# Performance work log

Measured on AMD Instinct MI355X. Metric: run time of the kernel, lower is better.

The kernel has to match this reference:

```python
import jax, jax.numpy as jnp
import numpy as np

DIM = 2048
K = 8                 # top_k
M = 16                # max_transients
BIND_FRAC = 0.15
BETA = 0.05
GAMMA = 0.9
LIFETIME = 5
B, T = 64, 256

_iu, _ju = np.triu_indices(K, k=1)   # row-major: matches torch's (ii outer, jj inner) loop order
IU = jnp.asarray(_iu, jnp.int32)
JU = jnp.asarray(_ju, jnp.int32)


def _renorm(s):
    n = jnp.sqrt(jnp.sum(jnp.abs(s) ** 2, axis=-1, keepdims=True))
    return s / jnp.maximum(n, 1e-8)


def setup_inputs() -> dict:
    key = jax.random.key(0)
    ks = jax.random.split(key, 5)
    return {
        "x": jax.random.normal(ks[0], (B, T, DIM), jnp.float32),
        "tape_re": jax.random.normal(ks[1], (DIM,), jnp.float32) / np.sqrt(DIM).astype(np.float32),
        "tape_im": jax.random.normal(ks[2], (DIM,), jnp.float32) / np.sqrt(DIM).astype(np.float32),
        "eta_param": jnp.asarray(0.1, jnp.float32),
        "torque_bias_re": jax.random.normal(ks[3], (DIM,), jnp.float32) * 0.01,
        "torque_bias_im": jax.random.normal(ks[4], (DIM,), jnp.float32) * 0.01,
    }


def _per_batch(h, s, ti, tj, mre, mim, cnt, eta, tbias):
    """One timestep for one batch element. s: [D] complex64, transients: 5 arrays of [M]."""
    c = h * s                               # Hadamard reception
    _, top_idx = jax.lax.top_k(jnp.abs(c), K)
    top_c = c[top_idx]
    tm = jnp.abs(top_c)
    ph = jnp.angle(top_c)
    # co-resonance scores for the K*(K-1)/2 pairs; torch detaches via .item()
    score = jax.lax.stop_gradient(tm[IU] * tm[JU] * jnp.cos(ph[IU] - ph[JU]))
    pos = score > 0
    n_pos = jnp.sum(pos.astype(jnp.int32))
    n_bind = jnp.maximum(1, (n_pos.astype(jnp.float32) * BIND_FRAC).astype(jnp.int32))
    sorted_desc = -jnp.sort(-jnp.where(pos, score, -jnp.inf))
    theta_idx = jnp.minimum(n_bind - 1, jnp.maximum(n_pos - 1, 0))
    theta = sorted_desc[theta_idx]
    bind = (score >= theta) & (n_pos > 0)   # theta>0 so only positive scores pass

    ci = top_idx[IU]
    cj = top_idx[JU]
    prod = s[ci] * s[cj]
    mnew = jax.lax.stop_gradient(BETA * prod / jnp.maximum(jnp.abs(prod), 1e-8))  # torch detaches via .item()

    def step(tr, inp):
        ti, tj, mre, mim, cnt = tr
        ci_p, cj_p, do, mr, mi = inp
        active = cnt > 0
        match = active & (((ti == ci_p) & (tj == cj_p)) | ((ti == cj_p) & (tj == ci_p)))
        has_match = jnp.any(match)
        midx = jnp.argmax(match)
        free = ~active
        has_free = jnp.any(free)
        fidx = jnp.argmax(free)
        refresh = do & has_match
        insert = do & (~has_match) & has_free
        cnt = jnp.where(refresh, cnt.at[midx].set(LIFETIME), cnt)
        ti = jnp.where(insert, ti.at[fidx].set(ci_p), ti)
        tj = jnp.where(insert, tj.at[fidx].set(cj_p), tj)
        mre = jnp.where(insert, mre.at[fidx].set(mr), mre)
        mim = jnp.where(insert, mim.at[fidx].set(mi), mim)
        cnt = jnp.where(insert, cnt.at[fidx].set(LIFETIME), cnt)
        return (ti, tj, mre, mim, cnt), None

    (ti, tj, mre, mim, cnt), _ = jax.lax.scan(
        step, (ti, tj, mre, mim, cnt), (ci, cj, bind, mnew.real, mnew.imag))

    # decay all transients
    mre = mre * GAMMA
    mim = mim * GAMMA
    cnt = cnt - 1
    alive = (cnt > 0) & (jnp.sqrt(mre * mre + mim * mim) > 1e-6)
    cnt = jnp.where(alive, cnt, 0)
    mre = jnp.where(alive, mre, 0.0)
    mim = jnp.where(alive, mim, 0.0)

    # augment state with transients (scatter-add to both endpoints)
    s_re = s.real.at[ti].add(0.1 * mre).at[tj].add(0.1 * mre)
    s_im = s.imag.at[ti].add(0.1 * mim).at[tj].add(0.1 * mim)
    s_aug = jax.lax.complex(s_re, s_im)

    c_aug = h * s_aug
    re_c = c_aug.real
    im_c = c_aug.imag
    res_mask = ((re_c > 1e-6) & (jnp.abs(im_c) < re_c)).astype(jnp.float32)
    tor_mask = ((re_c < -1e-6) | (jnp.abs(im_c) >= jnp.abs(re_c))).astype(jnp.float32)
    orth_mask = 1.0 - res_mask - tor_mask
    update = eta * (c_aug * (1.0 - orth_mask) + tor_mask * tbias)
    s_new = _renorm(s + update)
    return s_new, ti, tj, mre, mim, cnt


def _forward(x, tape_re, tape_im, eta_param, torque_bias_re, torque_bias_im):
    Bb, Tt, D = x.shape
    s0 = _renorm(jax.lax.complex(tape_re, tape_im)[None, :])
    s0 = jnp.broadcast_to(s0, (Bb, D))
    eta = jnp.abs(eta_param)
    tbias = jax.lax.complex(torque_bias_re, torque_bias_im)
    ti0 = jnp.zeros((Bb, M), jnp.int32)
    tj0 = jnp.zeros((Bb, M), jnp.int32)
    mre0 = jnp.zeros((Bb, M), jnp.float32)
    mim0 = jnp.zeros((Bb, M), jnp.float32)
    cnt0 = jnp.zeros((Bb, M), jnp.int32)

    step_b = jax.vmap(_per_batch, in_axes=(0, 0, 0, 0, 0, 0, 0, None, None))

    def time_step(carry, h_t):
        s, ti, tj, mre, mim, cnt = carry
        s, ti, tj, mre, mim, cnt = step_b(h_t, s, ti, tj, mre, mim, cnt, eta, tbias)
        return (s, ti, tj, mre, mim, cnt), jnp.abs(s)

    _, outs = jax.lax.scan(time_step, (s0, ti0, tj0, mre0, mim0, cnt0),
                           jnp.transpose(x, (1, 0, 2)))  # [T,B,D]
    return jnp.transpose(outs, (1, 0, 2))                # [B,T,D]


def reference(x, tape_re, tape_im, eta_param, torque_bias_re, torque_bias_im):
    return _forward(x, tape_re, tape_im, eta_param, torque_bias_re, torque_bias_im)
```

## Files before the change

### kernel.cpp

```cpp
#include <hip/hip_runtime.h>
#include <math.h>

#define DIM_ 2048
#define KTOP 8
#define MSLOT 16
#define TSTEPS 256
#define NB 64
#define NTHREADS 320
#define NWORK 256
#define EPT 8
#define CCAP 128

static_assert(NWORK * EPT == DIM_, "mapping");

#define DPP0(src, ctrl, rm) __builtin_amdgcn_update_dpp(0, (src), (ctrl), (rm), 0xf, true)

__device__ __forceinline__ void ced(double &a, double &b) {
  double mx = fmax(a, b);
  b = fmin(a, b);
  a = mx;
}

template <int CTRL, int RM>
__device__ __forceinline__ void merge_2to4_d(double k[8]) {
  int lo0 = DPP0(__double2loint(k[0]), CTRL, RM);
  int hi0 = DPP0(__double2hiint(k[0]), CTRL, RM);
  int lo1 = DPP0(__double2loint(k[1]), CTRL, RM);
  int hi1 = DPP0(__double2hiint(k[1]), CTRL, RM);
  double b0 = __hiloint2double(hi0, lo0);
  double b1 = __hiloint2double(hi1, lo1);
  double z2 = b1, z3 = b0;
  ced(k[0], z2); ced(k[1], z3);
  ced(k[0], k[1]); ced(z2, z3);
  k[2] = z2; k[3] = z3;
}

template <int CTRL, int RM>
__device__ __forceinline__ void merge_first4(double k[8]) {
  double b[4];
#pragma unroll
  for (int i = 0; i < 4; i++) {
    int lo = DPP0(__double2loint(k[i]), CTRL, RM);
    int hi = DPP0(__double2hiint(k[i]), CTRL, RM);
    b[i] = __hiloint2double(hi, lo);
  }
  k[4] = b[3]; k[5] = b[2]; k[6] = b[1]; k[7] = b[0];
  ced(k[0],k[4]); ced(k[1],k[5]); ced(k[2],k[6]); ced(k[3],k[7]);
  ced(k[0],k[2]); ced(k[1],k[3]); ced(k[4],k[6]); ced(k[5],k[7]);
  ced(k[0],k[1]); ced(k[2],k[3]); ced(k[4],k[5]); ced(k[6],k[7]);
}

template <int CTRL, int RM>
__device__ __forceinline__ void merge_level(double k[8]) {
  double b[8];
#pragma unroll
  for (int i = 0; i < 8; i++) {
    int lo = DPP0(__double2loint(k[i]), CTRL, RM);
    int hi = DPP0(__double2hiint(k[i]), CTRL, RM);
    b[i] = __hiloint2double(hi, lo);
  }
#pragma unroll
  for (int i = 0; i < 8; i++) k[i] = fmax(k[i], b[7 - i]);
  ced(k[0],k[4]); ced(k[1],k[5]); ced(k[2],k[6]); ced(k[3],k[7]);
  ced(k[0],k[2]); ced(k[1],k[3]); ced(k[4],k[6]); ced(k[5],k[7]);
  ced(k[0],k[1]); ced(k[2],k[3]); ced(k[4],k[5]); ced(k[6],k[7]);
}

__device__ __forceinline__ void cedf(float &a, float &b) {
  float mx = fmaxf(a, b);
  b = fminf(a, b);
  a = mx;
}
__device__ __forceinline__ void sort4f(float k[8]) {
  cedf(k[0],k[1]); cedf(k[2],k[3]);
  cedf(k[0],k[2]); cedf(k[1],k[3]);
  cedf(k[1],k[2]);
}
template <int CTRL, int RM>
__device__ __forceinline__ void merge_first4_f32(float k[8]) {
  float b[4];
#pragma unroll
  for (int i = 0; i < 4; i++)
    b[i] = __int_as_float(DPP0(__float_as_int(k[i]), CTRL, RM));
  k[4] = b[3]; k[5] = b[2]; k[6] = b[1]; k[7] = b[0];
  cedf(k[0],k[4]); cedf(k[1],k[5]); cedf(k[2],k[6]); cedf(k[3],k[7]);
  cedf(k[0],k[2]); cedf(k[1],k[3]); cedf(k[4],k[6]); cedf(k[5],k[7]);
  cedf(k[0],k[1]); cedf(k[2],k[3]); cedf(k[4],k[5]); cedf(k[6],k[7]);
}
template <int CTRL, int RM>
__device__ __forceinline__ void merge_level_f32(float k[8]) {
  float b[8];
#pragma unroll
  for (int i = 0; i < 8; i++)
    b[i] = __int_as_float(DPP0(__float_as_int(k[i]), CTRL, RM));
#pragma unroll
  for (int i = 0; i < 8; i++) k[i] = fmaxf(k[i], b[7 - i]);
  cedf(k[0],k[4]); cedf(k[1],k[5]); cedf(k[2],k[6]); cedf(k[3],k[7]);
  cedf(k[0],k[2]); cedf(k[1],k[3]); cedf(k[4],k[6]); cedf(k[5],k[7]);
  cedf(k[0],k[1]); cedf(k[2],k[3]); cedf(k[4],k[5]); cedf(k[6],k[7]);
}

#define FMAX_STAGE(x, ctrl, rm)                                                \
  x = fmaxf(x, __int_as_float(DPP0(__float_as_int(x), ctrl, rm)))
#define FADD_STAGE(x, ctrl, rm)                                                \
  x = x + __int_as_float(DPP0(__float_as_int(x), ctrl, rm))

__device__ __forceinline__ float wave_max_f32(float x) {
  FMAX_STAGE(x, 0x111, 0xf);
  FMAX_STAGE(x, 0x112, 0xf);
  FMAX_STAGE(x, 0x114, 0xf);
  FMAX_STAGE(x, 0x118, 0xf);
  FMAX_STAGE(x, 0x142, 0xa);
  FMAX_STAGE(x, 0x143, 0xc);
  return x;
}
__device__ __forceinline__ float wave_sum_f32(float x) {
  FADD_STAGE(x, 0x111, 0xf);
  FADD_STAGE(x, 0x112, 0xf);
  FADD_STAGE(x, 0x114, 0xf);
  FADD_STAGE(x, 0x118, 0xf);
  FADD_STAGE(x, 0x142, 0xa);
  FADD_STAGE(x, 0x143, 0xc);
  return x;
}
__device__ __forceinline__ int rl63(int v) {
  return __builtin_amdgcn_readlane(v, 63);
}

__global__ void __launch_bounds__(NTHREADS)
me_fused(const float *__restrict__ x, const float *__restrict__ tape_re,
         const float *__restrict__ tape_im, const float *__restrict__ eta_param,
         const float *__restrict__ tbias_re, const float *__restrict__ tbias_im,
         float *__restrict__ out) {
  __shared__ float4 sc4[DIM_];
  __shared__ float2 dxy[DIM_];
  __shared__ float4 lmax4[NWORK / 4];
  __shared__ unsigned long long cand_lds[CCAP];
  __shared__ int ccnt;
  __shared__ float red_sh[4];

  const int tid = threadIdx.x;
  const int lane = tid & 63;
  const int wid = tid >> 6;
  const int wtid = tid - 64;
  const int b = blockIdx.x;

  const float eta = fabsf(eta_param[0]);

  float vre[EPT], vim[EPT], tbre_[EPT], tbim_[EPT];
  float hcur[EPT], hnext[EPT], av[EPT];
  const float *xb = x + (size_t)b * TSTEPS * DIM_;

  if (wid > 0) {
    float acc = 0.f, lm = 0.f;
#pragma unroll
    for (int j = 0; j < EPT; j++) {
      int e = wtid + NWORK * j;
      float a = tape_re[e], c2 = tape_im[e];
      vre[j] = a; vim[j] = c2;
      tbre_[j] = tbias_re[e]; tbim_[j] = tbias_im[e];
      float h = xb[e];
      hcur[j] = h; hnext[j] = h;
      dxy[e] = make_float2(0.f, 0.f);
      acc += a * a + c2 * c2;
      float cr = h * a, ci = h * c2;
      av[j] = sqrtf(cr * cr + ci * ci);
      lm = fmaxf(lm, av[j]);
      sc4[e] = make_float4(h, a, c2, 0.f);
    }
    float ws = wave_sum_f32(acc);
    if (lane == 63) red_sh[wid - 1] = ws;
    ((float *)lmax4)[wtid] = lm;
  }
  if (tid == 0) ccnt = 0;

  int s_ti = 0, s_tj = 0, s_cnt = 0;
  float s_mre = 0.f, s_mim = 0.f;

  float osr[EPT], osi[EPT];

  __syncthreads();

  for (int t = 0; t < TSTEPS; t++) {
    float ivn;
    {
      float tot = (red_sh[0] + red_sh[1]) + (red_sh[2] + red_sh[3]);
      ivn = 1.f / fmaxf(sqrtf(tot), 1e-8f);
    }

    if (wid > 0) {
      float4 q = lmax4[lane];
      float k[8];
      k[0] = q.x; k[1] = q.y; k[2] = q.z; k[3] = q.w;
      k[4] = 0.f; k[5] = 0.f; k[6] = 0.f; k[7] = 0.f;
      sort4f(k);
      merge_first4_f32<0x111, 0xf>(k);
      merge_level_f32<0x112, 0xf>(k);
      merge_level_f32<0x114, 0xf>(k);
      merge_level_f32<0x118, 0xf>(k);
      merge_level_f32<0x142, 0xa>(k);
      merge_level_f32<0x143, 0xc>(k);
      float th = __int_as_float(rl63(__float_as_int(k[7])));
#pragma unroll
      for (int j = 0; j < EPT; j++) {
        if (av[j] >= th) {
          int e = wtid + NWORK * j;
          int slot = atomicAdd(&ccnt, 1);
          if (slot < CCAP)
            cand_lds[slot] = (unsigned long long)__double_as_longlong(
                __hiloint2double(__float_as_int(av[j]), ~e));
        }
      }
    }
    __syncthreads();

    if (wid == 0) {
      int cnt = ccnt;
      if (lane == 0) ccnt = 0;
      if (cnt > CCAP) cnt = CCAP;
      unsigned long long u0 = cand_lds[2 * lane];
      unsigned long long u1 = cand_lds[2 * lane + 1];
      double a = (2 * lane < cnt) ? __longlong_as_double((long long)u0) : 0.0;
      double b2 = (2 * lane + 1 < cnt) ? __longlong_as_double((long long)u1) : 0.0;
      double c[8];
      c[0] = fmax(a, b2); c[1] = fmin(a, b2);
      c[2] = 0.0; c[3] = 0.0; c[4] = 0.0; c[5] = 0.0; c[6] = 0.0; c[7] = 0.0;
      merge_2to4_d<0x111, 0xf>(c);
      merge_first4<0x112, 0xf>(c);
      int src = 3;
      if (cnt > 8)  { merge_level<0x114, 0xf>(c); src = 7;  }
      if (cnt > 16) { merge_level<0x118, 0xf>(c); src = 15; }
      if (cnt > 32) { merge_level<0x142, 0xa>(c); src = 31; }
      if (cnt > 64) { merge_level<0x143, 0xc>(c); src = 63; }
      int top[KTOP];
#pragma unroll
      for (int r = 0; r < KTOP; r++)
        top[r] = ~__builtin_amdgcn_readlane(__double2loint(c[r]), src);

      int pi = (lane < 28) ? lane : 27;
      int ii = 0, base = 0;
      if (pi >= 7)  { ii = 1; base = 7;  }
      if (pi >= 13) { ii = 2; base = 13; }
      if (pi >= 18) { ii = 3; base = 18; }
      if (pi >= 22) { ii = 4; base = 22; }
      if (pi >= 25) { ii = 5; base = 25; }
      if (pi >= 27) { ii = 6; base = 27; }
      int jj = ii + 1 + (pi - base);
      int gi = top[0];
      if (ii == 1) gi = top[1];
      if (ii == 2) gi = top[2];
      if (ii == 3) gi = top[3];
      if (ii == 4) gi = top[4];
      if (ii == 5) gi = top[5];
      if (ii == 6) gi = top[6];
      int gj = top[1];
      if (jj == 2) gj = top[2];
      if (jj == 3) gj = top[3];
      if (jj == 4) gj = top[4];
      if (jj == 5) gj = top[5];
      if (jj == 6) gj = top[6];
      if (jj == 7) gj = top[7];

      float4 c4i = sc4[gi], c4j = sc4[gj];
      float sri = c4i.y * ivn, sii2 = c4i.z * ivn;
      float srj = c4j.y * ivn, sij = c4j.z * ivn;
      float cri = c4i.x * sri, cii = c4i.x * sii2;
      float crj = c4j.x * srj, cij = c4j.x * sij;
      float score = cri * crj + cii * cij;
      bool valid = (lane < 28);
      bool pos = valid && (score > 0.f);
      unsigned long long posmask = __ballot(pos);
      int npos = __popcll(posmask);
      float pr = sri * srj - sii2 * sij;
      float pq = sri * sij + sii2 * srj;
      float ap = fmaxf(sqrtf(pr * pr + pq * pq), 1e-8f);
      float mr = (0.05f * pr) / ap, mi = (0.05f * pq) / ap;

      unsigned long long bmask = 0ull;
      if (npos > 0) {
        int nbind = (int)((float)npos * 0.15f);
        if (nbind < 1) nbind = 1;
        float val = pos ? score : -__builtin_inff();
        float th2 = 0.f;
        for (int k2 = 0; k2 < nbind; ++k2) {
          float mx = wave_max_f32(val);
          th2 = __int_as_float(rl63(__float_as_int(mx)));
          if (k2 + 1 < nbind) {
            unsigned long long em = __ballot(val == th2);
            if (lane == (int)__builtin_ctzll(em)) val = -__builtin_inff();
          }
        }
        bool bind = valid && (score >= th2);
        bmask = __ballot(bind);
      }
      while (bmask) {
        int pp = (int)__builtin_ctzll(bmask);
        bmask &= bmask - 1;
        int pci = __builtin_amdgcn_readlane(gi, pp);
        int pcj = __builtin_amdgcn_readlane(gj, pp);
        int pmr = __builtin_amdgcn_readlane(__float_as_int(mr), pp);
        int pmi = __builtin_amdgcn_readlane(__float_as_int(mi), pp);
        bool isslot = (lane < MSLOT);
        bool match = isslot && (s_cnt > 0) &&
                     ((s_ti == pci && s_tj == pcj) ||
                      (s_ti == pcj && s_tj == pci));
        unsigned long long mm = __ballot(match);
        if (mm != 0ull) {
          if (lane == (int)__builtin_ctzll(mm)) s_cnt = 5;
        } else {
          unsigned long long fm = __ballot(isslot && s_cnt <= 0);
          if (fm != 0ull && lane == (int)__builtin_ctzll(fm)) {
            s_ti = pci; s_tj = pcj;
            s_mre = __int_as_float(pmr); s_mim = __int_as_float(pmi);
            s_cnt = 5;
          }
        }
      }
      if (lane < MSLOT) {
        s_mre *= 0.9f; s_mim *= 0.9f; s_cnt -= 1;
        bool alive = (s_cnt > 0) &&
                     (sqrtf(s_mre * s_mre + s_mim * s_mim) > 1e-6f);
        if (!alive) { s_cnt = 0; s_mre = 0.f; s_mim = 0.f; }
        if (s_cnt > 0) {
          atomicAdd(&dxy[s_ti].x, 0.1f * s_mre);
          atomicAdd(&dxy[s_tj].x, 0.1f * s_mre);
          atomicAdd(&dxy[s_ti].y, 0.1f * s_mim);
          atomicAdd(&dxy[s_tj].y, 0.1f * s_mim);
        }
      }
    } else {
      if (t + 1 < TSTEPS) {
        const float *xr = xb + (size_t)(t + 1) * DIM_;
#pragma unroll
        for (int j = 0; j < EPT; j++) hnext[j] = xr[wtid + NWORK * j];
      }
      if (t > 0) {
        float *op = out + ((size_t)b * TSTEPS + (t - 1)) * DIM_;
#pragma unroll
        for (int j = 0; j < EPT; j++) {
          float sr = vre[j] * ivn, si = vim[j] * ivn;
          op[wtid + NWORK * j] = sqrtf(sr * sr + si * si);
        }
      }
#pragma unroll
      for (int j = 0; j < EPT; j++) {
        float sri = vre[j] * ivn, sii2 = vim[j] * ivn;
        osr[j] = sri; osi[j] = sii2;
        float h = hcur[j];
        float car = h * sri, cai = h * sii2;
        bool res = (car > 1e-6f) && (fabsf(cai) < car);
        bool tor = (car < -1e-6f) || (fabsf(cai) >= fabsf(car));
        float m1 = (res || tor) ? 1.f : 0.f;
        float mt = tor ? 1.f : 0.f;
        float ur = eta * (car * m1 + mt * tbre_[j]);
        float ui = eta * (cai * m1 + mt * tbim_[j]);
        vre[j] = sri + ur; vim[j] = sii2 + ui;
      }
    }
    __syncthreads();

    if (wid > 0) {
      float2 dd[EPT];
#pragma unroll
      for (int j = 0; j < EPT; j++) dd[j] = dxy[wtid + NWORK * j];
      float acc2 = 0.f, lm = 0.f;
#pragma unroll
      for (int j = 0; j < EPT; j++) {
        int e = wtid + NWORK * j;
        if (dd[j].x != 0.f || dd[j].y != 0.f) {
          dxy[e] = make_float2(0.f, 0.f);
          float ar = osr[j] + dd[j].x, ai = osi[j] + dd[j].y;
          float h = hcur[j];
          float car = h * ar, cai = h * ai;
          bool res = (car > 1e-6f) && (fabsf(cai) < car);
          bool tor = (car < -1e-6f) || (fabsf(cai) >= fabsf(car));
          float m1 = (res || tor) ? 1.f : 0.f;
          float mt = tor ? 1.f : 0.f;
          float ur = eta * (car * m1 + mt * tbre_[j]);
          float ui = eta * (cai * m1 + mt * tbim_[j]);
          vre[j] = osr[j] + ur; vim[j] = osi[j] + ui;
        }
        acc2 += vre[j] * vre[j] + vim[j] * vim[j];
        float h = hnext[j];
        hcur[j] = h;
        float cr = h * vre[j], ci = h * vim[j];
        av[j] = sqrtf(cr * cr + ci * ci);
        lm = fmaxf(lm, av[j]);
        sc4[e] = make_float4(h, vre[j], vim[j], 0.f);
      }
      float ws = wave_sum_f32(acc2);
      if (lane == 63) red_sh[wid - 1] = ws;
      ((float *)lmax4)[wtid] = lm;
    }
    __syncthreads();
  }

  if (wid > 0) {
    float tot = (red_sh[0] + red_sh[1]) + (red_sh[2] + red_sh[3]);
    float ivnF = 1.f / fmaxf(sqrtf(tot), 1e-8f);
    float *op = out + ((size_t)b * TSTEPS + (TSTEPS - 1)) * DIM_;
#pragma unroll
    for (int j = 0; j < EPT; j++) {
      float sr = vre[j] * ivnF, si = vim[j] * ivnF;
      op[wtid + NWORK * j] = sqrtf(sr * sr + si * si);
    }
  }
}

extern "C" void kernel_launch(void *const *d_in, const int *in_sizes, int n_in,
                              void *d_out, int out_size, void *d_ws,
                              size_t ws_size, hipStream_t stream) {
  const float *x = (const float *)d_in[0];
  const float *tre = (const float *)d_in[1];
  const float *tim = (const float *)d_in[2];
  const float *eta = (const float *)d_in[3];
  const float *tbre = (const float *)d_in[4];
  const float *tbim = (const float *)d_in[5];
  float *out = (float *)d_out;
  me_fused<<<NB, NTHREADS, 0, stream>>>(x, tre, tim, eta, tbre, tbim, out);
}
```

Measured before the change: 1.038 ms.

## Compute per-wave candidate thresholds and double-buffer state to drop a barrier

Each worker wave now computes its top-8 threshold from its own lanes' maxima and emits candidates at the end of the update phase. This replaces the block-wide lmax4 merge that needed its own __syncthreads at the start of each timestep. The sc4 state array is double-buffered, and the next step's magnitudes are computed speculatively in the worker phase, so the selection wave and the updates no longer race. This removes one barrier per timestep, at the cost of more candidates (up to about 32+) for wave 0 to merge and some duplicated magnitude work.

Result: slower. 1.137 ms (+9.5%).

```diff
diff --git a/kernel.cpp b/kernel.cpp
--- a/kernel.cpp
+++ b/kernel.cpp
@@ -71,11 +71,6 @@
   b = fminf(a, b);
   a = mx;
 }
-__device__ __forceinline__ void sort4f(float k[8]) {
-  cedf(k[0],k[1]); cedf(k[2],k[3]);
-  cedf(k[0],k[2]); cedf(k[1],k[3]);
-  cedf(k[1],k[2]);
-}
 template <int CTRL, int RM>
 __device__ __forceinline__ void merge_first4_f32(float k[8]) {
   float b[4];
@@ -127,14 +122,39 @@
   return __builtin_amdgcn_readlane(v, 63);
 }
 
+__device__ __forceinline__ float wave_theta8(float lm) {
+  float k[8];
+  k[0] = lm;
+#pragma unroll
+  for (int i = 1; i < 8; i++) k[i] = 0.f;
+  {
+    float b0 = __int_as_float(DPP0(__float_as_int(k[0]), 0x111, 0xf));
+    float mx = fmaxf(k[0], b0);
+    k[1] = fminf(k[0], b0);
+    k[0] = mx;
+  }
+  {
+    float b0 = __int_as_float(DPP0(__float_as_int(k[0]), 0x112, 0xf));
+    float b1 = __int_as_float(DPP0(__float_as_int(k[1]), 0x112, 0xf));
+    float z2 = b1, z3 = b0;
+    cedf(k[0], z2); cedf(k[1], z3);
+    cedf(k[0], k[1]); cedf(z2, z3);
+    k[2] = z2; k[3] = z3;
+  }
+  merge_first4_f32<0x114, 0xf>(k);
+  merge_level_f32<0x118, 0xf>(k);
+  merge_level_f32<0x142, 0xa>(k);
+  merge_level_f32<0x143, 0xc>(k);
+  return __int_as_float(rl63(__float_as_int(k[7])));
+}
+
 __global__ void __launch_bounds__(NTHREADS)
 me_fused(const float *__restrict__ x, const float *__restrict__ tape_re,
          const float *__restrict__ tape_im, const float *__restrict__ eta_param,
          const float *__restrict__ tbias_re, const float *__restrict__ tbias_im,
          float *__restrict__ out) {
-  __shared__ float4 sc4[DIM_];
+  __shared__ float4 sc4[2][DIM_];
   __shared__ float2 dxy[DIM_];
-  __shared__ float4 lmax4[NWORK / 4];
   __shared__ unsigned long long cand_lds[CCAP];
   __shared__ int ccnt;
   __shared__ float red_sh[4];
@@ -149,10 +169,13 @@
 
   float vre[EPT], vim[EPT], tbre_[EPT], tbim_[EPT];
   float hcur[EPT], hnext[EPT], av[EPT];
+  float osr[EPT], osi[EPT];
   const float *xb = x + (size_t)b * TSTEPS * DIM_;
 
+  if (tid == 0) ccnt = 0;
+  float lm0 = 0.f;
   if (wid > 0) {
-    float acc = 0.f, lm = 0.f;
+    float acc = 0.f;
 #pragma unroll
     for (int j = 0; j < EPT; j++) {
       int e = wtid + NWORK * j;
@@ -165,21 +188,32 @@
       acc += a * a + c2 * c2;
       float cr = h * a, ci = h * c2;
       av[j] = sqrtf(cr * cr + ci * ci);
-      lm = fmaxf(lm, av[j]);
-      sc4[e] = make_float4(h, a, c2, 0.f);
+      lm0 = fmaxf(lm0, av[j]);
+      sc4[0][e] = make_float4(h, a, c2, 0.f);
     }
     float ws = wave_sum_f32(acc);
     if (lane == 63) red_sh[wid - 1] = ws;
-    ((float *)lmax4)[wtid] = lm;
-  }
-  if (tid == 0) ccnt = 0;
+  }
+  __syncthreads();
+  if (wid > 0) {
+    float th = wave_theta8(lm0);
+#pragma unroll
+    for (int j = 0; j < EPT; j++) {
+      if (av[j] >= th) {
+        int e = wtid + NWORK * j;
+        int slot = atomicAdd(&ccnt, 1);
+        if (slot < CCAP)
+          cand_lds[slot] = (unsigned long long)__double_as_longlong(
+              __hiloint2double(__float_as_int(av[j]), ~e));
+      }
+    }
+  }
 
   int s_ti = 0, s_tj = 0, s_cnt = 0;
   float s_mre = 0.f, s_mim = 0.f;
 
-  float osr[EPT], osi[EPT];
-
   __syncthreads();
+  int buf = 0;
 
   for (int t = 0; t < TSTEPS; t++) {
     float ivn;
@@ -187,32 +221,6 @@
       float tot = (red_sh[0] + red_sh[1]) + (red_sh[2] + red_sh[3]);
       ivn = 1.f / fmaxf(sqrtf(tot), 1e-8f);
     }
-
-    if (wid > 0) {
-      float4 q = lmax4[lane];
-      float k[8];
-      k[0] = q.x; k[1] = q.y; k[2] = q.z; k[3] = q.w;
-      k[4] = 0.f; k[5] = 0.f; k[6] = 0.f; k[7] = 0.f;
-      sort4f(k);
-      merge_first4_f32<0x111, 0xf>(k);
-      merge_level_f32<0x112, 0xf>(k);
-      merge_level_f32<0x114, 0xf>(k);
-      merge_level_f32<0x118, 0xf>(k);
-      merge_level_f32<0x142, 0xa>(k);
-      merge_level_f32<0x143, 0xc>(k);
-      float th = __int_as_float(rl63(__float_as_int(k[7])));
-#pragma unroll
-      for (int j = 0; j < EPT; j++) {
-        if (av[j] >= th) {
-          int e = wtid + NWORK * j;
-          int slot = atomicAdd(&ccnt, 1);
-          if (slot < CCAP)
-            cand_lds[slot] = (unsigned long long)__double_as_longlong(
-                __hiloint2double(__float_as_int(av[j]), ~e));
-        }
-      }
-    }
-    __syncthreads();
 
     if (wid == 0) {
       int cnt = ccnt;
@@ -261,7 +269,7 @@
       if (jj == 6) gj = top[6];
       if (jj == 7) gj = top[7];
 
-      float4 c4i = sc4[gi], c4j = sc4[gj];
+      float4 c4i = sc4[buf][gi], c4j = sc4[buf][gj];
       float sri = c4i.y * ivn, sii2 = c4i.z * ivn;
       float srj = c4j.y * ivn, sij = c4j.z * ivn;
       float cri = c4i.x * sri, cii = c4i.x * sii2;
@@ -334,18 +342,19 @@
 #pragma unroll
         for (int j = 0; j < EPT; j++) hnext[j] = xr[wtid + NWORK * j];
       }
+#pragma unroll
+      for (int j = 0; j < EPT; j++) {
+        osr[j] = vre[j] * ivn; osi[j] = vim[j] * ivn;
+      }
       if (t > 0) {
         float *op = out + ((size_t)b * TSTEPS + (t - 1)) * DIM_;
 #pragma unroll
-        for (int j = 0; j < EPT; j++) {
-          float sr = vre[j] * ivn, si = vim[j] * ivn;
-          op[wtid + NWORK * j] = sqrtf(sr * sr + si * si);
-        }
+        for (int j = 0; j < EPT; j++)
+          op[wtid + NWORK * j] = sqrtf(osr[j] * osr[j] + osi[j] * osi[j]);
       }
 #pragma unroll
       for (int j = 0; j < EPT; j++) {
-        float sri = vre[j] * ivn, sii2 = vim[j] * ivn;
-        osr[j] = sri; osi[j] = sii2;
+        float sri = osr[j], sii2 = osi[j];
         float h = hcur[j];
         float car = h * sri, cai = h * sii2;
         bool res = (car > 1e-6f) && (fabsf(cai) < car);
@@ -355,6 +364,14 @@
         float ur = eta * (car * m1 + mt * tbre_[j]);
         float ui = eta * (cai * m1 + mt * tbim_[j]);
         vre[j] = sri + ur; vim[j] = sii2 + ui;
+      }
+#pragma unroll
+      for (int j = 0; j < EPT; j++) {
+        int e = wtid + NWORK * j;
+        float h2 = hnext[j];
+        float cr = h2 * vre[j], ci = h2 * vim[j];
+        av[j] = sqrtf(cr * cr + ci * ci);
+        sc4[buf ^ 1][e] = make_float4(h2, vre[j], vim[j], 0.f);
       }
     }
     __syncthreads();
@@ -379,20 +396,31 @@
           float ur = eta * (car * m1 + mt * tbre_[j]);
           float ui = eta * (cai * m1 + mt * tbim_[j]);
           vre[j] = osr[j] + ur; vim[j] = osi[j] + ui;
+          float h2 = hnext[j];
+          float cr = h2 * vre[j], ci = h2 * vim[j];
+          av[j] = sqrtf(cr * cr + ci * ci);
+          sc4[buf ^ 1][e] = make_float4(h2, vre[j], vim[j], 0.f);
         }
         acc2 += vre[j] * vre[j] + vim[j] * vim[j];
-        float h = hnext[j];
-        hcur[j] = h;
-        float cr = h * vre[j], ci = h * vim[j];
-        av[j] = sqrtf(cr * cr + ci * ci);
         lm = fmaxf(lm, av[j]);
-        sc4[e] = make_float4(h, vre[j], vim[j], 0.f);
+        hcur[j] = hnext[j];
       }
       float ws = wave_sum_f32(acc2);
       if (lane == 63) red_sh[wid - 1] = ws;
-      ((float *)lmax4)[wtid] = lm;
+      float th = wave_theta8(lm);
+#pragma unroll
+      for (int j = 0; j < EPT; j++) {
+        if (av[j] >= th) {
+          int e = wtid + NWORK * j;
+          int slot = atomicAdd(&ccnt, 1);
+          if (slot < CCAP)
+            cand_lds[slot] = (unsigned long long)__double_as_longlong(
+                __hiloint2double(__float_as_int(av[j]), ~e));
+        }
+      }
     }
     __syncthreads();
+    buf ^= 1;
   }
 
   if (wid > 0) {
```

## Widen block to eight worker waves with four elements per thread

Applied to the files above, without the earlier changes.

Doubles the worker wavefronts from four to eight, so each thread handles four state elements instead of eight. The per-wave max reduction now reads two lmax4 entries and starts from a full 8-element sort network instead of a padded 4-sort, and the norm reduction sums eight partials. The scaled state is computed once and reused for the output write. The aim is to shorten each thread's serial per-timestep work on the single-block-per-batch recurrence, at the cost of more waves joining each barrier.

Measured after the change: 1.052 ms. About the same (+1.3%).

```diff
diff --git a/kernel.cpp b/kernel.cpp
--- a/kernel.cpp
+++ b/kernel.cpp
@@ -6,9 +6,9 @@
 #define MSLOT 16
 #define TSTEPS 256
 #define NB 64
-#define NTHREADS 320
-#define NWORK 256
-#define EPT 8
+#define NTHREADS 576
+#define NWORK 512
+#define EPT 4
 #define CCAP 128
 
 static_assert(NWORK * EPT == DIM_, "mapping");
@@ -71,21 +71,13 @@
   b = fminf(a, b);
   a = mx;
 }
-__device__ __forceinline__ void sort4f(float k[8]) {
-  cedf(k[0],k[1]); cedf(k[2],k[3]);
-  cedf(k[0],k[2]); cedf(k[1],k[3]);
-  cedf(k[1],k[2]);
-}
-template <int CTRL, int RM>
-__device__ __forceinline__ void merge_first4_f32(float k[8]) {
-  float b[4];
-#pragma unroll
-  for (int i = 0; i < 4; i++)
-    b[i] = __int_as_float(DPP0(__float_as_int(k[i]), CTRL, RM));
-  k[4] = b[3]; k[5] = b[2]; k[6] = b[1]; k[7] = b[0];
+__device__ __forceinline__ void sort8f(float k[8]) {
+  cedf(k[0],k[1]); cedf(k[2],k[3]); cedf(k[4],k[5]); cedf(k[6],k[7]);
+  cedf(k[0],k[2]); cedf(k[1],k[3]); cedf(k[4],k[6]); cedf(k[5],k[7]);
+  cedf(k[1],k[2]); cedf(k[5],k[6]);
   cedf(k[0],k[4]); cedf(k[1],k[5]); cedf(k[2],k[6]); cedf(k[3],k[7]);
-  cedf(k[0],k[2]); cedf(k[1],k[3]); cedf(k[4],k[6]); cedf(k[5],k[7]);
-  cedf(k[0],k[1]); cedf(k[2],k[3]); cedf(k[4],k[5]); cedf(k[6],k[7]);
+  cedf(k[2],k[4]); cedf(k[3],k[5]);
+  cedf(k[1],k[2]); cedf(k[3],k[4]); cedf(k[5],k[6]);
 }
 template <int CTRL, int RM>
 __device__ __forceinline__ void merge_level_f32(float k[8]) {
@@ -137,7 +129,7 @@
   __shared__ float4 lmax4[NWORK / 4];
   __shared__ unsigned long long cand_lds[CCAP];
   __shared__ int ccnt;
-  __shared__ float red_sh[4];
+  __shared__ float red_sh[8];
 
   const int tid = threadIdx.x;
   const int lane = tid & 63;
@@ -149,6 +141,7 @@
 
   float vre[EPT], vim[EPT], tbre_[EPT], tbim_[EPT];
   float hcur[EPT], hnext[EPT], av[EPT];
+  float osr[EPT], osi[EPT];
   const float *xb = x + (size_t)b * TSTEPS * DIM_;
 
   if (wid > 0) {
@@ -177,24 +170,24 @@
   int s_ti = 0, s_tj = 0, s_cnt = 0;
   float s_mre = 0.f, s_mim = 0.f;
 
-  float osr[EPT], osi[EPT];
-
   __syncthreads();
 
   for (int t = 0; t < TSTEPS; t++) {
     float ivn;
     {
-      float tot = (red_sh[0] + red_sh[1]) + (red_sh[2] + red_sh[3]);
+      float tot = ((red_sh[0] + red_sh[1]) + (red_sh[2] + red_sh[3])) +
+                  ((red_sh[4] + red_sh[5]) + (red_sh[6] + red_sh[7]));
       ivn = 1.f / fmaxf(sqrtf(tot), 1e-8f);
     }
 
     if (wid > 0) {
-      float4 q = lmax4[lane];
+      float4 qa = lmax4[lane];
+      float4 qb = lmax4[64 + lane];
       float k[8];
-      k[0] = q.x; k[1] = q.y; k[2] = q.z; k[3] = q.w;
-      k[4] = 0.f; k[5] = 0.f; k[6] = 0.f; k[7] = 0.f;
-      sort4f(k);
-      merge_first4_f32<0x111, 0xf>(k);
+      k[0] = qa.x; k[1] = qa.y; k[2] = qa.z; k[3] = qa.w;
+      k[4] = qb.x; k[5] = qb.y; k[6] = qb.z; k[7] = qb.w;
+      sort8f(k);
+      merge_level_f32<0x111, 0xf>(k);
       merge_level_f32<0x112, 0xf>(k);
       merge_level_f32<0x114, 0xf>(k);
       merge_level_f32<0x118, 0xf>(k);
@@ -334,18 +327,19 @@
 #pragma unroll
         for (int j = 0; j < EPT; j++) hnext[j] = xr[wtid + NWORK * j];
       }
+#pragma unroll
+      for (int j = 0; j < EPT; j++) {
+        osr[j] = vre[j] * ivn; osi[j] = vim[j] * ivn;
+      }
       if (t > 0) {
         float *op = out + ((size_t)b * TSTEPS + (t - 1)) * DIM_;
 #pragma unroll
-        for (int j = 0; j < EPT; j++) {
-          float sr = vre[j] * ivn, si = vim[j] * ivn;
-          op[wtid + NWORK * j] = sqrtf(sr * sr + si * si);
-        }
+        for (int j = 0; j < EPT; j++)
+          op[wtid + NWORK * j] = sqrtf(osr[j] * osr[j] + osi[j] * osi[j]);
       }
 #pragma unroll
       for (int j = 0; j < EPT; j++) {
-        float sri = vre[j] * ivn, sii2 = vim[j] * ivn;
-        osr[j] = sri; osi[j] = sii2;
+        float sri = osr[j], sii2 = osi[j];
         float h = hcur[j];
         float car = h * sri, cai = h * sii2;
         bool res = (car > 1e-6f) && (fabsf(cai) < car);
@@ -396,7 +390,8 @@
   }
 
   if (wid > 0) {
-    float tot = (red_sh[0] + red_sh[1]) + (red_sh[2] + red_sh[3]);
+    float tot = ((red_sh[0] + red_sh[1]) + (red_sh[2] + red_sh[3])) +
+                ((red_sh[4] + red_sh[5]) + (red_sh[6] + red_sh[7]));
     float ivnF = 1.f / fmaxf(sqrtf(tot), 1e-8f);
     float *op = out + ((size_t)b * TSTEPS + (TSTEPS - 1)) * DIM_;
 #pragma unroll
```
